# Kernel optimization log

Hardware: AMD Instinct MI355X
Metric: run time of the kernel (lower is better)

## Reference

```python
import jax, jax.numpy as jnp
import numpy as np

B, H, W = 2, 128, 128
MID = 64            # mid_channels
DG = 16             # deform_groups
MAX_RES = 10.0      # max_residue_magnitude
CIN_OFF = 3 * MID + 4   # 196: cat(extra_feat, flow_1, flow_2)
COFF = DG * 27          # 432: o1 + o2 + mask, each DG*9


def setup_inputs() -> dict:
    key = jax.random.key(0)
    ks = jax.random.split(key, 9)
    return {
        "extra_feat": jax.random.normal(ks[0], (B, 3 * MID, H, W), jnp.float32),
        "flow_1": jax.random.normal(ks[1], (B, 2, H, W), jnp.float32) * 2.0,
        "flow_2": jax.random.normal(ks[2], (B, 2, H, W), jnp.float32) * 2.0,
        "feat_prop": jax.random.normal(ks[3], (B, MID, H, W), jnp.float32),
        "feat_n2": jax.random.normal(ks[4], (B, MID, H, W), jnp.float32),
        "w_off": jax.random.normal(ks[5], (COFF, CIN_OFF, 3, 3), jnp.float32) * 0.02,
        "b_off": jax.random.normal(ks[6], (COFF,), jnp.float32) * 0.02,
        "dc_weight": jax.random.normal(ks[7], (MID, 2 * MID, 3, 3), jnp.float32) * 0.05,
        "dc_bias": jax.random.normal(ks[8], (MID,), jnp.float32) * 0.05,
    }


def _conv3x3(x, w, b):
    y = jax.lax.conv_general_dilated(
        x, w, window_strides=(1, 1), padding=((1, 1), (1, 1)),
        dimension_numbers=("NCHW", "OIHW", "NCHW"))
    return y + b[None, :, None, None]


def _deform_conv2d(inp, offset, mask, weight, bias):
    # inp: [B, Cin, H, W]; offset: [B, 2*DG*9, H, W] (per group, per kernel pos: (dy, dx));
    # mask: [B, DG*9, H, W]; weight: [Cout, Cin, 3, 3]; stride=1, pad=1, dil=1.
    Bb, Cin, Hi, Wi = inp.shape
    K = 9
    cg = Cin // DG
    Ho, Wo = Hi, Wi
    ki = jnp.repeat(jnp.arange(3), 3)  # kernel row index per flat k (row-major)
    kj = jnp.tile(jnp.arange(3), 3)
    base_y = (jnp.arange(Ho) - 1)[None, :, None] + ki[:, None, None]  # [K, Ho, 1]
    base_x = (jnp.arange(Wo) - 1)[None, None, :] + kj[:, None, None]  # [K, 1, Wo]
    off = offset.reshape(Bb, DG, K, 2, Ho, Wo)
    py = base_y[None, None] + off[:, :, :, 0]  # [B, DG, K, Ho, Wo]
    px = base_x[None, None] + off[:, :, :, 1]
    y0 = jnp.floor(py)
    x0 = jnp.floor(px)
    inp_g = inp.reshape(Bb, DG, cg, Hi * Wi)
    acc = jnp.zeros((Bb, DG, cg, K, Ho, Wo), inp.dtype)
    for dy in (0.0, 1.0):
        for dx in (0.0, 1.0):
            yc = y0 + dy
            xc = x0 + dx
            wgt = (1.0 - jnp.abs(py - yc)) * (1.0 - jnp.abs(px - xc))
            valid = (yc >= 0) & (yc < Hi) & (xc >= 0) & (xc < Wi)
            idx = (jnp.clip(yc, 0, Hi - 1) * Wi + jnp.clip(xc, 0, Wi - 1)).astype(jnp.int32)
            idx = jnp.broadcast_to(idx.reshape(Bb, DG, 1, K * Ho * Wo), (Bb, DG, cg, K * Ho * Wo))
            g = jnp.take_along_axis(inp_g, idx, axis=3).reshape(Bb, DG, cg, K, Ho, Wo)
            acc = acc + g * (wgt * valid)[:, :, None]
    sm = acc * mask.reshape(Bb, DG, 1, K, Ho, Wo)  # modulated samples
    wr = weight.reshape(weight.shape[0], DG, cg, K)
    out = jnp.einsum("bgckhw,ogck->bohw", sm, wr) + bias[None, :, None, None]
    return out


def reference(extra_feat, flow_1, flow_2, feat_prop, feat_n2, w_off, b_off, dc_weight, dc_bias):
    x = jnp.concatenate([extra_feat, flow_1, flow_2], axis=1)
    out = _conv3x3(x, w_off, b_off)
    o1, o2, m = jnp.split(out, 3, axis=1)  # each [B, DG*9, H, W]
    offset = MAX_RES * jnp.tanh(jnp.concatenate([o1, o2], axis=1))
    rep = DG * 3 * 3 // 2  # 72
    f1 = jnp.tile(flow_1[:, ::-1], (1, rep, 1, 1))  # flip(1): (dx,dy)->(dy,dx)
    f2 = jnp.tile(flow_2[:, ::-1], (1, rep, 1, 1))
    half = offset.shape[1] // 2
    offset = jnp.concatenate([offset[:, :half] + f1, offset[:, half:] + f2], axis=1)
    mask = jax.nn.sigmoid(m)
    inp = jnp.concatenate([feat_prop, feat_n2], axis=1)
    return _deform_conv2d(inp, offset, mask, dc_weight, dc_bias)
```

## Files before the change

kernel.cpp:

```cpp
#include <hip/hip_runtime.h>
#include <math.h>

#define Hh 128
#define Ww 128
#define HW (128*128)
#define CIN_OFF 196
#define COFF 432

typedef _Float16 half8 __attribute__((ext_vector_type(8)));
typedef _Float16 half4 __attribute__((ext_vector_type(4)));
typedef _Float16 half2v __attribute__((ext_vector_type(2)));
typedef float f32x4 __attribute__((ext_vector_type(4)));

static __device__ __forceinline__ half8 splat8(float v) {
  _Float16 h = (_Float16)v;
  half8 r = {h, h, h, h, h, h, h, h};
  return r;
}

__global__ __launch_bounds__(256) void k_prep_dcw(const float* __restrict__ dcw,
                                                  _Float16* __restrict__ wH) {
  int idx = blockIdx.x * 256 + threadIdx.x;
  if (idx < 64 * 1152) {
    int co = idx / 1152;
    int j  = idx - co * 1152;
    int k  = j >> 7;
    int ci = j & 127;
    wH[idx] = (_Float16)dcw[(co * 128 + ci) * 9 + k];
  }
}

__global__ __launch_bounds__(256) void k_prep_w(const float* __restrict__ w_off,
                                                _Float16* __restrict__ BpT,
                                                _Float16* __restrict__ Bt) {
  int idx = blockIdx.x * 256 + threadIdx.x;
  if (idx < 774144) {
    const int c  = idx & 7;
    const int n  = (idx >> 3) % 448;
    const int sl = (idx >> 3) / 448;
    const int l4 = sl & 3;
    const int s  = sl >> 2;
    const int t  = s / 6;
    const int cg = s - t * 6;
    const int ci = cg * 32 + l4 * 8 + c;
    BpT[idx] = (_Float16)((n < COFF) ? w_off[((size_t)n * CIN_OFF + ci) * 9 + t] : 0.f);
  } else if (idx < 774144 + 16128) {
    const int j = idx - 774144;
    const int c = j & 3;
    const int n = (j >> 2) % 448;
    const int t = (j >> 2) / 448;
    Bt[j] = (_Float16)((n < COFF) ? w_off[((size_t)n * CIN_OFF + 192 + c) * 9 + t] : 0.f);
  }
}

__global__ __launch_bounds__(256) void k_prep_feat(const float* __restrict__ fp,
                                                   const float* __restrict__ fn2,
                                                   _Float16* __restrict__ featT) {
  const int t = blockIdx.x * 256 + threadIdx.x;
  const int b = t >> 14;
  const int hw = t & 16383;
#pragma unroll
  for (int g = 0; g < 16; ++g) {
    const float* src = (g < 8) ? fp : fn2;
    const int ch0 = (g & 7) * 8;
    half8 v;
#pragma unroll
    for (int c = 0; c < 8; ++c)
      v[c] = (_Float16)src[(size_t)(b * 64 + ch0 + c) * HW + hw];
    *(half8*)(featT + (((size_t)(b * 16 + g)) * HW + hw) * 8) = v;
  }
}

__global__ __launch_bounds__(512, 2) void k_offconv_mfma(
    const float* __restrict__ extra, const float* __restrict__ f1, const float* __restrict__ f2,
    const _Float16* __restrict__ BpT, const _Float16* __restrict__ Bt,
    const float* __restrict__ b_off,
    float* __restrict__ off_pm, _Float16* __restrict__ mask_pm) {
  __shared__ __align__(16) _Float16 smA[3 * 130 * 192];
  __shared__ __align__(16) _Float16 smT[3 * 130 * 4];
  const int h    = blockIdx.x;
  const int b    = blockIdx.y;
  const int tid  = (int)threadIdx.x;
  const int lane = tid & 63;
  const int wid  = tid >> 6;
  const int wm   = wid >> 2;
  const int wn   = wid & 3;
  const int m_base = wm * 64;
  const int n_base = wn * 112;
  const int l15 = lane & 15;
  const int l4  = lane >> 4;

  for (int z = tid; z < 588; z += 512) {
    const int p2 = z % 98;
    const int rr = z / 98;
    const int r  = (rr >= 3) ? (rr - 3) : rr;
    const int px = (rr >= 3) ? 129 : 0;
    if (p2 < 96) {
      const int ci = 2 * p2, biw = ci >> 3;
      const int sw = ((biw & 24) | ((biw & 7) ^ (px & 7))) << 3;
      *(half2v*)(smA + (r * 130 + px) * 192 + sw + (ci & 7)) = (half2v){(_Float16)0.f, (_Float16)0.f};
    } else {
      *(half2v*)(smT + (r * 130 + px) * 4 + 2 * (p2 - 96)) = (half2v){(_Float16)0.f, (_Float16)0.f};
    }
  }

  for (int task = tid; task < 9408; task += 512) {
    const int q  = task & 31;
    const int rp = task >> 5;
    const int p2 = rp % 98;
    const int r  = rp / 98;
    const int gh = h - 1 + r;
    const int ci = 2 * p2;
    float4 va = {0.f, 0.f, 0.f, 0.f}, vb = va;
    if ((unsigned)gh < (unsigned)Hh) {
      const float* xpA;
      if (p2 < 96)       xpA = extra + (size_t)(b * 192 + ci) * HW;
      else if (p2 == 96) xpA = f1 + (size_t)(b * 2) * HW;
      else               xpA = f2 + (size_t)(b * 2) * HW;
      va = *(const float4*)(xpA + gh * Ww + 4 * q);
      vb = *(const float4*)(xpA + HW + gh * Ww + 4 * q);
    }
    const float av[4] = {va.x, va.y, va.z, va.w};
    const float bv[4] = {vb.x, vb.y, vb.z, vb.w};
    if (p2 < 96) {
      const int biw = ci >> 3;
#pragma unroll
      for (int i = 0; i < 4; ++i) {
        const int px = 1 + 4 * q + i;
        const int sw = ((biw & 24) | ((biw & 7) ^ (px & 7))) << 3;
        half2v pk; pk[0] = (_Float16)av[i]; pk[1] = (_Float16)bv[i];
        *(half2v*)(smA + (r * 130 + px) * 192 + sw + (ci & 7)) = pk;
      }
    } else {
      const int ct = 2 * (p2 - 96);
#pragma unroll
      for (int i = 0; i < 4; ++i) {
        const int px = 1 + 4 * q + i;
        half2v pk; pk[0] = (_Float16)av[i]; pk[1] = (_Float16)bv[i];
        *(half2v*)(smT + (r * 130 + px) * 4 + ct) = pk;
      }
    }
  }
  __syncthreads();

  f32x4 acc[4][7];
#pragma unroll
  for (int i = 0; i < 4; ++i)
#pragma unroll
    for (int j = 0; j < 7; ++j) acc[i][j] = (f32x4){0.f, 0.f, 0.f, 0.f};

  const bool lz = (l4 == 0);
#pragma unroll 3
  for (int t = 0; t < 9; ++t) {
    const int ki = t / 3;
    const int kj = t - 3 * ki;
#pragma unroll
    for (int cg = 0; cg < 6; ++cg) {
      const int s4 = ((t * 6 + cg) * 4 + l4) * 448;
      half8 bf[7];
#pragma unroll
      for (int f = 0; f < 7; ++f)
        bf[f] = *(const half8*)(BpT + (size_t)(s4 + n_base + f * 16 + l15) * 8);
      half8 af[4];
#pragma unroll
      for (int mf = 0; mf < 4; ++mf) {
        const int px = m_base + mf * 16 + l15 + kj;
        const int bi = cg * 4 + l4;
        af[mf] = *(const half8*)(smA + (ki * 130 + px) * 192 +
                                 (((bi & 24) | ((bi & 7) ^ (px & 7))) << 3));
      }
#pragma unroll
      for (int mf = 0; mf < 4; ++mf)
#pragma unroll
        for (int f = 0; f < 7; ++f)
          acc[mf][f] = __builtin_amdgcn_mfma_f32_16x16x32_f16(af[mf], bf[f], acc[mf][f], 0, 0, 0);
    }
    half8 aft[4];
#pragma unroll
    for (int mf = 0; mf < 4; ++mf) {
      const int px = m_base + mf * 16 + l15 + kj;
      const half4 tv = *(const half4*)(smT + (ki * 130 + px) * 4);
      half8 a = {0, 0, 0, 0, 0, 0, 0, 0};
      if (lz) { a[0] = tv[0]; a[1] = tv[1]; a[2] = tv[2]; a[3] = tv[3]; }
      aft[mf] = a;
    }
#pragma unroll
    for (int f = 0; f < 7; ++f) {
      const half4 wv = *(const half4*)(Bt + (size_t)(t * 448 + n_base + f * 16 + l15) * 4);
      half8 bb = {0, 0, 0, 0, 0, 0, 0, 0};
      if (lz) { bb[0] = wv[0]; bb[1] = wv[1]; bb[2] = wv[2]; bb[3] = wv[3]; }
#pragma unroll
      for (int mf = 0; mf < 4; ++mf)
        acc[mf][f] = __builtin_amdgcn_mfma_f32_16x16x32_f16(aft[mf], bb, acc[mf][f], 0, 0, 0);
    }
  }

  const int hw0 = h * Ww;
#pragma unroll
  for (int f = 0; f < 7; ++f) {
    const int n = n_base + f * 16 + l15;
    if (n >= COFF) continue;
    const float bias = b_off[n];
    const bool isOff = (n < 288);
    const float* fl = (n < 144) ? f1 : f2;
    const size_t fladd = (size_t)(b * 2 + ((n & 1) ^ 1)) * HW;
#pragma unroll
    for (int mf = 0; mf < 4; ++mf) {
#pragma unroll
      for (int rr = 0; rr < 4; ++rr) {
        const int m = m_base + mf * 16 + l4 * 4 + rr;
        const float v = acc[mf][f][rr] + bias;
        const int p = hw0 + m;
        if (isOff) {
          off_pm[((size_t)b * HW + p) * 288 + n] = 10.f * tanhf(v) + fl[fladd + p];
        } else {
          mask_pm[((size_t)b * HW + p) * 144 + (n - 288)] = (_Float16)(1.f / (1.f + expf(-v)));
        }
      }
    }
  }
}

__global__ __launch_bounds__(256) void k_deform2(
    const _Float16* __restrict__ featT, const float* __restrict__ off_pm,
    const _Float16* __restrict__ mask_pm, const _Float16* __restrict__ wH,
    const float* __restrict__ dcb, float* __restrict__ out) {
  __shared__ __align__(16) char smem[16 * 1160 * 2];
  _Float16* sm = (_Float16*)smem;
  float* red = (float*)smem;
  const int w0  = blockIdx.x * 16;
  const int h   = blockIdx.y;
  const int b   = blockIdx.z;
  const int tid = (int)threadIdx.x;
  const int lane = tid & 63, wid = tid >> 6;
  const int l15 = lane & 15, l4 = lane >> 4;

#pragma unroll 1
  for (int i = 0; i < 9; ++i) {
    const int p   = tid + i * 256;
    const int pix = p / 144;
    const int r   = p - pix * 144;
    const int g   = r / 9;
    const int k   = r - g * 9;
    const int w   = w0 + pix;
    const int hw  = h * Ww + w;
    const float2 off = *(const float2*)(off_pm + ((size_t)b * HW + hw) * 288 + 2 * r);
    const float mk = (float)mask_pm[((size_t)b * HW + hw) * 144 + r];
    const int ki = (k >= 6) ? 2 : (k >= 3 ? 1 : 0);
    const int kj = k - 3 * ki;
    const float py = (float)(h - 1 + ki) + off.x;
    const float px = (float)(w - 1 + kj) + off.y;
    const float y0f = floorf(py), x0f = floorf(px);
    const int y0 = (int)y0f, x0 = (int)x0f;
    const float ly = py - y0f, lx = px - x0f;
    const float hy = 1.f - ly, hx = 1.f - lx;
    const int y1 = y0 + 1, x1 = x0 + 1;
    const bool vy0 = (unsigned)y0 < (unsigned)Hh, vy1 = (unsigned)y1 < (unsigned)Hh;
    const bool vx0 = (unsigned)x0 < (unsigned)Ww, vx1 = (unsigned)x1 < (unsigned)Ww;
    const float w00 = (vy0 && vx0) ? hy * hx : 0.f;
    const float w01 = (vy0 && vx1) ? hy * lx : 0.f;
    const float w10 = (vy1 && vx0) ? ly * hx : 0.f;
    const float w11 = (vy1 && vx1) ? ly * lx : 0.f;
    const int cy0 = min(max(y0, 0), Hh - 1), cy1 = min(max(y1, 0), Hh - 1);
    const int cx0 = min(max(x0, 0), Ww - 1), cx1 = min(max(x1, 0), Ww - 1);
    const _Float16* gbase = featT + ((size_t)(b * 16 + g) * HW) * 8;
    const half8 s00 = *(const half8*)(gbase + (cy0 * Ww + cx0) * 8);
    const half8 s01 = *(const half8*)(gbase + (cy0 * Ww + cx1) * 8);
    const half8 s10 = *(const half8*)(gbase + (cy1 * Ww + cx0) * 8);
    const half8 s11 = *(const half8*)(gbase + (cy1 * Ww + cx1) * 8);
    half8 v = s00 * splat8(w00) + s01 * splat8(w01) + s10 * splat8(w10) + s11 * splat8(w11);
    v = v * splat8(mk);
    const int swz = (g ^ (k & 7)) << 3;
    *(half8*)(sm + pix * 1160 + k * 128 + swz) = v;
  }
  __syncthreads();

  f32x4 acc[4];
#pragma unroll
  for (int nf = 0; nf < 4; ++nf) acc[nf] = (f32x4){0.f, 0.f, 0.f, 0.f};
#pragma unroll
  for (int j = 0; j < 9; ++j) {
    const int s  = wid * 9 + j;
    const int k  = s >> 2;
    const int cg = s & 3;
    const int gidx = cg * 4 + l4;
    const half8 af = *(const half8*)(sm + l15 * 1160 + k * 128 + ((gidx ^ (k & 7)) << 3));
    const int koff = s * 32 + l4 * 8;
#pragma unroll
    for (int nf = 0; nf < 4; ++nf) {
      const half8 bf = *(const half8*)(wH + (nf * 16 + l15) * 1152 + koff);
      acc[nf] = __builtin_amdgcn_mfma_f32_16x16x32_f16(af, bf, acc[nf], 0, 0, 0);
    }
  }
  __syncthreads();
#pragma unroll
  for (int nf = 0; nf < 4; ++nf)
#pragma unroll
    for (int rr = 0; rr < 4; ++rr)
      red[(wid * 16 + l4 * 4 + rr) * 66 + nf * 16 + l15] = acc[nf][rr];
  __syncthreads();

  const int m  = tid & 15;
  const int ng = tid >> 4;
#pragma unroll
  for (int i = 0; i < 4; ++i) {
    const int n = ng + 16 * i;
    float val = red[(0 * 16 + m) * 66 + n] + red[(1 * 16 + m) * 66 + n] +
                red[(2 * 16 + m) * 66 + n] + red[(3 * 16 + m) * 66 + n];
    out[(size_t)(b * 64 + n) * HW + h * Ww + w0 + m] = val + dcb[n];
  }
}

extern "C" void kernel_launch(void* const* d_in, const int* in_sizes, int n_in,
                              void* d_out, int out_size, void* d_ws, size_t ws_size,
                              hipStream_t stream) {
  const float* extra = (const float*)d_in[0];
  const float* f1    = (const float*)d_in[1];
  const float* f2    = (const float*)d_in[2];
  const float* fp    = (const float*)d_in[3];
  const float* fn2   = (const float*)d_in[4];
  const float* w_off = (const float*)d_in[5];
  const float* b_off = (const float*)d_in[6];
  const float* dcw   = (const float*)d_in[7];
  const float* dcb   = (const float*)d_in[8];
  float* out = (float*)d_out;

  float*    off_pm  = (float*)d_ws;
  _Float16* mask_pm = (_Float16*)(off_pm + 2 * 288 * HW);
  _Float16* featT   = mask_pm + 2 * 144 * HW;
  _Float16* BpT     = featT + 2 * 128 * HW;
  _Float16* Bt      = BpT + 774144;
  _Float16* wH      = Bt + 16128;

  hipLaunchKernelGGL(k_prep_dcw, dim3(288), dim3(256), 0, stream, dcw, wH);
  hipLaunchKernelGGL(k_prep_w, dim3((774144 + 16128 + 255) / 256), dim3(256), 0, stream,
                     w_off, BpT, Bt);
  hipLaunchKernelGGL(k_prep_feat, dim3(128), dim3(256), 0, stream, fp, fn2, featT);
  hipLaunchKernelGGL(k_offconv_mfma, dim3(128, 2), dim3(512), 0, stream,
                     extra, f1, f2, BpT, Bt, b_off, off_pm, mask_pm);
  hipLaunchKernelGGL(k_deform2, dim3(8, 128, 2), dim3(256), 0, stream,
                     featT, off_pm, mask_pm, wH, dcb, out);
}
```

Measured before the change: 203.1 us.

## Double offset-conv block to 1024 threads, split M per wave, use fast exp

The offset-conv kernel now runs 1024 threads per block, so each wave handles 32 output pixels instead of 64 and holds half as many accumulators. The goal is more waves in flight to hide latency. The staging loop is remapped so each of 9 iterations loads only the extra_feat channels with a coalescing-friendly index order, and a separate small pass loads the flow channels. tanh and sigmoid switch to __expf-based formulas, which are cheaper but slightly less accurate. B-fragment global loads are now issued twice as often per output, since twice as many waves reload the same weights.

Result: faster. 190.6 us (-6.2%).

```diff
diff --git a/kernel.cpp b/kernel.cpp
--- a/kernel.cpp
+++ b/kernel.cpp
@@ -71,7 +71,7 @@
   }
 }
 
-__global__ __launch_bounds__(512, 2) void k_offconv_mfma(
+__global__ __launch_bounds__(1024, 4) void k_offconv_mfma(
     const float* __restrict__ extra, const float* __restrict__ f1, const float* __restrict__ f2,
     const _Float16* __restrict__ BpT, const _Float16* __restrict__ Bt,
     const float* __restrict__ b_off,
@@ -85,14 +85,14 @@
   const int wid  = tid >> 6;
   const int wm   = wid >> 2;
   const int wn   = wid & 3;
-  const int m_base = wm * 64;
+  const int m_base = wm * 32;
   const int n_base = wn * 112;
   const int l15 = lane & 15;
   const int l4  = lane >> 4;
 
-  for (int z = tid; z < 588; z += 512) {
-    const int p2 = z % 98;
-    const int rr = z / 98;
+  if (tid < 588) {
+    const int p2 = tid % 98;
+    const int rr = tid / 98;
     const int r  = (rr >= 3) ? (rr - 3) : rr;
     const int px = (rr >= 3) ? 129 : 0;
     if (p2 < 96) {
@@ -104,48 +104,62 @@
     }
   }
 
-  for (int task = tid; task < 9408; task += 512) {
-    const int q  = task & 31;
-    const int rp = task >> 5;
-    const int p2 = rp % 98;
-    const int r  = rp / 98;
-    const int gh = h - 1 + r;
-    const int ci = 2 * p2;
+#pragma unroll 1
+  for (int j = 0; j < 9; ++j) {
+    const int J   = tid + 1024 * j;
+    const int p2a = J & 15;
+    const int qa  = (J >> 4) & 3;
+    const int R   = J >> 6;
+    const int r   = R / 48;
+    const int rem = R - 48 * r;
+    const int qh  = rem & 7;
+    const int p2h = rem >> 3;
+    const int q   = qa + 4 * qh;
+    const int p2  = p2a + 16 * p2h;
+    const int ci  = 2 * p2;
+    const int gh  = h - 1 + r;
     float4 va = {0.f, 0.f, 0.f, 0.f}, vb = va;
     if ((unsigned)gh < (unsigned)Hh) {
-      const float* xpA;
-      if (p2 < 96)       xpA = extra + (size_t)(b * 192 + ci) * HW;
-      else if (p2 == 96) xpA = f1 + (size_t)(b * 2) * HW;
-      else               xpA = f2 + (size_t)(b * 2) * HW;
-      va = *(const float4*)(xpA + gh * Ww + 4 * q);
-      vb = *(const float4*)(xpA + HW + gh * Ww + 4 * q);
+      const float* xp = extra + (size_t)(b * 192 + ci) * HW + gh * Ww + 4 * q;
+      va = *(const float4*)xp;
+      vb = *(const float4*)(xp + HW);
     }
     const float av[4] = {va.x, va.y, va.z, va.w};
     const float bv[4] = {vb.x, vb.y, vb.z, vb.w};
-    if (p2 < 96) {
-      const int biw = ci >> 3;
-#pragma unroll
-      for (int i = 0; i < 4; ++i) {
-        const int px = 1 + 4 * q + i;
-        const int sw = ((biw & 24) | ((biw & 7) ^ (px & 7))) << 3;
-        half2v pk; pk[0] = (_Float16)av[i]; pk[1] = (_Float16)bv[i];
-        *(half2v*)(smA + (r * 130 + px) * 192 + sw + (ci & 7)) = pk;
-      }
-    } else {
-      const int ct = 2 * (p2 - 96);
-#pragma unroll
-      for (int i = 0; i < 4; ++i) {
-        const int px = 1 + 4 * q + i;
-        half2v pk; pk[0] = (_Float16)av[i]; pk[1] = (_Float16)bv[i];
-        *(half2v*)(smT + (r * 130 + px) * 4 + ct) = pk;
-      }
+    const int biw = p2 >> 2;
+#pragma unroll
+    for (int i = 0; i < 4; ++i) {
+      const int px = 1 + 4 * q + i;
+      const int sw = ((biw & 24) | ((biw & 7) ^ (px & 7))) << 3;
+      half2v pk; pk[0] = (_Float16)av[i]; pk[1] = (_Float16)bv[i];
+      *(half2v*)(smA + (r * 130 + px) * 192 + sw + (ci & 7)) = pk;
+    }
+  }
+  if (tid < 192) {
+    const int q   = tid & 31;
+    const int p2t = (tid >> 5) & 1;
+    const int r   = tid >> 6;
+    const int gh  = h - 1 + r;
+    float4 va = {0.f, 0.f, 0.f, 0.f}, vb = va;
+    if ((unsigned)gh < (unsigned)Hh) {
+      const float* xp = (p2t ? f2 : f1) + (size_t)(b * 2) * HW + gh * Ww + 4 * q;
+      va = *(const float4*)xp;
+      vb = *(const float4*)(xp + HW);
+    }
+    const float av[4] = {va.x, va.y, va.z, va.w};
+    const float bv[4] = {vb.x, vb.y, vb.z, vb.w};
+#pragma unroll
+    for (int i = 0; i < 4; ++i) {
+      const int px = 1 + 4 * q + i;
+      half2v pk; pk[0] = (_Float16)av[i]; pk[1] = (_Float16)bv[i];
+      *(half2v*)(smT + (r * 130 + px) * 4 + 2 * p2t) = pk;
     }
   }
   __syncthreads();
 
-  f32x4 acc[4][7];
-#pragma unroll
-  for (int i = 0; i < 4; ++i)
+  f32x4 acc[2][7];
+#pragma unroll
+  for (int i = 0; i < 2; ++i)
 #pragma unroll
     for (int j = 0; j < 7; ++j) acc[i][j] = (f32x4){0.f, 0.f, 0.f, 0.f};
 
@@ -161,23 +175,23 @@
 #pragma unroll
       for (int f = 0; f < 7; ++f)
         bf[f] = *(const half8*)(BpT + (size_t)(s4 + n_base + f * 16 + l15) * 8);
-      half8 af[4];
-#pragma unroll
-      for (int mf = 0; mf < 4; ++mf) {
+      half8 af[2];
+#pragma unroll
+      for (int mf = 0; mf < 2; ++mf) {
         const int px = m_base + mf * 16 + l15 + kj;
         const int bi = cg * 4 + l4;
         af[mf] = *(const half8*)(smA + (ki * 130 + px) * 192 +
                                  (((bi & 24) | ((bi & 7) ^ (px & 7))) << 3));
       }
 #pragma unroll
-      for (int mf = 0; mf < 4; ++mf)
+      for (int mf = 0; mf < 2; ++mf)
 #pragma unroll
         for (int f = 0; f < 7; ++f)
           acc[mf][f] = __builtin_amdgcn_mfma_f32_16x16x32_f16(af[mf], bf[f], acc[mf][f], 0, 0, 0);
     }
-    half8 aft[4];
-#pragma unroll
-    for (int mf = 0; mf < 4; ++mf) {
+    half8 aft[2];
+#pragma unroll
+    for (int mf = 0; mf < 2; ++mf) {
       const int px = m_base + mf * 16 + l15 + kj;
       const half4 tv = *(const half4*)(smT + (ki * 130 + px) * 4);
       half8 a = {0, 0, 0, 0, 0, 0, 0, 0};
@@ -190,7 +204,7 @@
       half8 bb = {0, 0, 0, 0, 0, 0, 0, 0};
       if (lz) { bb[0] = wv[0]; bb[1] = wv[1]; bb[2] = wv[2]; bb[3] = wv[3]; }
 #pragma unroll
-      for (int mf = 0; mf < 4; ++mf)
+      for (int mf = 0; mf < 2; ++mf)
         acc[mf][f] = __builtin_amdgcn_mfma_f32_16x16x32_f16(aft[mf], bb, acc[mf][f], 0, 0, 0);
     }
   }
@@ -205,16 +219,18 @@
     const float* fl = (n < 144) ? f1 : f2;
     const size_t fladd = (size_t)(b * 2 + ((n & 1) ^ 1)) * HW;
 #pragma unroll
-    for (int mf = 0; mf < 4; ++mf) {
+    for (int mf = 0; mf < 2; ++mf) {
 #pragma unroll
       for (int rr = 0; rr < 4; ++rr) {
         const int m = m_base + mf * 16 + l4 * 4 + rr;
         const float v = acc[mf][f][rr] + bias;
         const int p = hw0 + m;
         if (isOff) {
-          off_pm[((size_t)b * HW + p) * 288 + n] = 10.f * tanhf(v) + fl[fladd + p];
+          const float e = __expf(2.f * v);
+          off_pm[((size_t)b * HW + p) * 288 + n] = 10.f * (1.f - 2.f / (e + 1.f)) + fl[fladd + p];
         } else {
-          mask_pm[((size_t)b * HW + p) * 144 + (n - 288)] = (_Float16)(1.f / (1.f + expf(-v)));
+          mask_pm[((size_t)b * HW + p) * 144 + (n - 288)] =
+              (_Float16)(1.f / (1.f + __expf(-v)));
         }
       }
     }
@@ -336,7 +352,7 @@
   hipLaunchKernelGGL(k_prep_w, dim3((774144 + 16128 + 255) / 256), dim3(256), 0, stream,
                      w_off, BpT, Bt);
   hipLaunchKernelGGL(k_prep_feat, dim3(128), dim3(256), 0, stream, fp, fn2, featT);
-  hipLaunchKernelGGL(k_offconv_mfma, dim3(128, 2), dim3(512), 0, stream,
+  hipLaunchKernelGGL(k_offconv_mfma, dim3(128, 2), dim3(1024), 0, stream,
                      extra, f1, f2, BpT, Bt, b_off, off_pm, mask_pm);
   hipLaunchKernelGGL(k_deform2, dim3(8, 128, 2), dim3(256), 0, stream,
                      featT, off_pm, mask_pm, wH, dcb, out);
```
